# Kernel optimization log

Hardware: AMD Instinct MI355X
Metric: run time of the kernel (lower is better)

Reference implementation:

```python
import jax, jax.numpy as jnp
import numpy as np

LN_EPS = 1e-5
N, D = 512, 512


def setup_inputs() -> dict:
    key = jax.random.key(0)
    ks = jax.random.split(key, 3)
    s1 = 1.0 / np.sqrt(2 * D)  # torch Linear default-ish scale
    s2 = 1.0 / np.sqrt(D)
    return {
        "embeddings": jax.random.normal(ks[0], (N, D), jnp.float32),
        "W1": jax.random.normal(ks[1], (2 * D, D), jnp.float32) * s1,  # [in, out]
        "b1": jnp.zeros((D,), jnp.float32),
        "gamma": jnp.ones((D,), jnp.float32),
        "beta": jnp.zeros((D,), jnp.float32),
        "W2": jax.random.normal(ks[2], (D, 1), jnp.float32) * s2,
        "b2": jnp.zeros((1,), jnp.float32),
    }


def reference(embeddings, W1, b1, gamma, beta, W2, b2):
    d = embeddings.shape[-1]
    # Linear(2D -> D) on cat(e_i, e_j) decomposes into two GEMMs + broadcast add,
    # avoiding materializing the [N, N, 2D] concatenated pair tensor.
    left = embeddings @ W1[:d]              # [N, D]  (contribution of e_i)
    right = embeddings @ W1[d:] + b1        # [N, D]  (contribution of e_j + bias)
    h = left[:, None, :] + right[None, :, :]  # [N, N, D]
    # LayerNorm over last dim (eps matches torch default)
    mu = h.mean(axis=-1, keepdims=True)
    var = ((h - mu) ** 2).mean(axis=-1, keepdims=True)
    h = (h - mu) * jax.lax.rsqrt(var + LN_EPS) * gamma + beta
    # exact GELU (torch nn.GELU default)
    h = jax.nn.gelu(h, approximate=False)
    s = jax.nn.sigmoid(jnp.squeeze(h @ W2, -1) + b2[0])  # [N, N]
    # original loop only evaluates pairs i <= j and mirrors to (j, i)
    n = s.shape[0]
    upper = jnp.arange(n)[:, None] <= jnp.arange(n)[None, :]
    return jnp.where(upper, s, s.T)
```

## Files before the change

kernel.cpp:

```cpp
#include <hip/hip_runtime.h>


#define N_ 512
#define D_ 512

__global__ __launch_bounds__(256) void k_gemm(const float* __restrict__ E,
                                              const float* __restrict__ W1,
                                              const float* __restrict__ b1,
                                              float* __restrict__ W ) {
    __shared__ float e[16][516];
    const int t = threadIdx.x;
    const int cc = (blockIdx.x & 7) * 128;
    const int r0 = (blockIdx.x >> 3) * 16;
    const int half = cc >> 9;
    const int c = (cc & 511) + (t & 31) * 4;
    const int rp = (t >> 5) * 2;

    for (int x = t; x < 16 * 128; x += 256) {
        int r = x >> 7, c4 = (x & 127) << 2;
        *(float4*)&e[r][c4] = *(const float4*)&E[(r0 + r) * D_ + c4];
    }
    __syncthreads();

    const float* __restrict__ wp = W1 + (half << 18) + c;
    float4 a0 = {0.f, 0.f, 0.f, 0.f}, a1 = {0.f, 0.f, 0.f, 0.f};
#pragma unroll 4
    for (int k = 0; k < D_; k += 4) {
        float4 e0 = *(float4*)&e[rp][k];
        float4 e1 = *(float4*)&e[rp + 1][k];
        float4 wa = *(const float4*)(wp + ((k + 0) << 9));
        float4 wb = *(const float4*)(wp + ((k + 1) << 9));
        float4 wc = *(const float4*)(wp + ((k + 2) << 9));
        float4 wd = *(const float4*)(wp + ((k + 3) << 9));
        a0.x = fmaf(e0.x, wa.x, a0.x); a0.y = fmaf(e0.x, wa.y, a0.y);
        a0.z = fmaf(e0.x, wa.z, a0.z); a0.w = fmaf(e0.x, wa.w, a0.w);
        a1.x = fmaf(e1.x, wa.x, a1.x); a1.y = fmaf(e1.x, wa.y, a1.y);
        a1.z = fmaf(e1.x, wa.z, a1.z); a1.w = fmaf(e1.x, wa.w, a1.w);
        a0.x = fmaf(e0.y, wb.x, a0.x); a0.y = fmaf(e0.y, wb.y, a0.y);
        a0.z = fmaf(e0.y, wb.z, a0.z); a0.w = fmaf(e0.y, wb.w, a0.w);
        a1.x = fmaf(e1.y, wb.x, a1.x); a1.y = fmaf(e1.y, wb.y, a1.y);
        a1.z = fmaf(e1.y, wb.z, a1.z); a1.w = fmaf(e1.y, wb.w, a1.w);
        a0.x = fmaf(e0.z, wc.x, a0.x); a0.y = fmaf(e0.z, wc.y, a0.y);
        a0.z = fmaf(e0.z, wc.z, a0.z); a0.w = fmaf(e0.z, wc.w, a0.w);
        a1.x = fmaf(e1.z, wc.x, a1.x); a1.y = fmaf(e1.z, wc.y, a1.y);
        a1.z = fmaf(e1.z, wc.z, a1.z); a1.w = fmaf(e1.z, wc.w, a1.w);
        a0.x = fmaf(e0.w, wd.x, a0.x); a0.y = fmaf(e0.w, wd.y, a0.y);
        a0.z = fmaf(e0.w, wd.z, a0.z); a0.w = fmaf(e0.w, wd.w, a0.w);
        a1.x = fmaf(e1.w, wd.x, a1.x); a1.y = fmaf(e1.w, wd.y, a1.y);
        a1.z = fmaf(e1.w, wd.z, a1.z); a1.w = fmaf(e1.w, wd.w, a1.w);
    }
    if (half) {
        float4 bb = *(const float4*)(b1 + c);
        a0.x += bb.x; a0.y += bb.y; a0.z += bb.z; a0.w += bb.w;
        a1.x += bb.x; a1.y += bb.y; a1.z += bb.z; a1.w += bb.w;
    }
    *(float4*)(W + ((half << 9) + r0 + rp) * D_ + c) = a0;
    *(float4*)(W + ((half << 9) + r0 + rp + 1) * D_ + c) = a1;
}

__global__ __launch_bounds__(256) void k_center(float* __restrict__ W,
                                                float* __restrict__ var) {
    const int t = threadIdx.x;
    const int lane = t & 63;
    const int r = (blockIdx.x << 2) + (t >> 6);
    float* p = W + r * D_;
    float4 v0 = *(float4*)&p[lane << 2];
    float4 v1 = *(float4*)&p[256 + (lane << 2)];
    float s = (v0.x + v0.y) + (v0.z + v0.w) + (v1.x + v1.y) + (v1.z + v1.w);
#pragma unroll
    for (int off = 32; off > 0; off >>= 1) s += __shfl_xor(s, off, 64);
    const float mean = s * (1.f / D_);
    v0.x -= mean; v0.y -= mean; v0.z -= mean; v0.w -= mean;
    v1.x -= mean; v1.y -= mean; v1.z -= mean; v1.w -= mean;
    float ss = v0.x * v0.x + v0.y * v0.y + v0.z * v0.z + v0.w * v0.w +
               v1.x * v1.x + v1.y * v1.y + v1.z * v1.z + v1.w * v1.w;
#pragma unroll
    for (int off = 32; off > 0; off >>= 1) ss += __shfl_xor(ss, off, 64);
    *(float4*)&p[lane << 2] = v0;
    *(float4*)&p[256 + (lane << 2)] = v1;
    if (lane == 0) var[r] = ss * (1.f / D_);
}


#define GELU1(L, R, G, BE, WC, RST, ACC)                                      \
    do {                                                                      \
        float s_ = (L) + (R);                                                 \
        float x_ = fmaf(s_ * (RST), (G), (BE));                               \
        float q_ = x_ * fmaf(-0.10294340f, x_ * x_, -2.30220935f);            \
        float e_ = __builtin_amdgcn_exp2f(q_);                                \
        float ge_ = x_ * __builtin_amdgcn_rcpf(1.f + e_);                     \
        ACC = fmaf(ge_, (WC), ACC);                                           \
    } while (0)

#define GELU4(LQ, RQ, RST, ACC)                                               \
    do {                                                                      \
        GELU1(LQ.x, RQ.x, g4.x, be4.x, w4.x, RST, ACC);                       \
        GELU1(LQ.y, RQ.y, g4.y, be4.y, w4.y, RST, ACC);                       \
        GELU1(LQ.z, RQ.z, g4.z, be4.z, w4.z, RST, ACC);                       \
        GELU1(LQ.w, RQ.w, g4.w, be4.w, w4.w, RST, ACC);                       \
    } while (0)

#define DOT4(LQ, RQ, ACC)                                                     \
    ACC += LQ.x * RQ.x + LQ.y * RQ.y + LQ.z * RQ.z + LQ.w * RQ.w

#define BFLY(V)                                                               \
    do {                                                                      \
        V += __shfl_xor(V, 1, 64);                                            \
        V += __shfl_xor(V, 2, 64);                                            \
        V += __shfl_xor(V, 4, 64);                                            \
        V += __shfl_xor(V, 8, 64);                                            \
    } while (0)

__global__ __launch_bounds__(512, 4) void k_pair(const float* __restrict__ W,
                                                 const float* __restrict__ var,
                                                 const float* __restrict__ gf,
                                                 const float* __restrict__ bef,
                                                 const float* __restrict__ wf,
                                                 const float* __restrict__ b2f,
                                                 float* __restrict__ out) {
    __shared__ float ls[16][516];
    __shared__ float rs[16][516];

    const int b = blockIdx.x;
    int I = (int)((65.0f - sqrtf(4225.0f - 8.0f * (float)b)) * 0.5f);
    if (I < 0) I = 0;
    if (I > 31) I = 31;
#define S_(i) (32 * (i) - ((i) * ((i)-1)) / 2)
    while (S_(I) > b) --I;
    while (S_(I + 1) <= b) ++I;
    const int J = I + (b - S_(I));
#undef S_

    const int t = threadIdx.x;
    const int ks = t & 15;
    const int pt = t >> 4;
    const int i2 = (pt & 7) * 2, j4 = (pt >> 3) * 4;
    const int Ibase = I * 16, Jbase = N_ + J * 16;

    for (int x = t; x < 16 * 128; x += 512) {
        int r = x >> 7, c4 = (x & 127) << 2;
        *(float4*)&ls[r][c4] = *(const float4*)&W[(Ibase + r) * D_ + c4];
        *(float4*)&rs[r][c4] = *(const float4*)&W[(Jbase + r) * D_ + c4];
    }
    __syncthreads();

    float cv0 = 0.f, cv1 = 0.f, cv2 = 0.f, cv3 = 0.f;
    float cv4 = 0.f, cv5 = 0.f, cv6 = 0.f, cv7 = 0.f;
    for (int it = 0; it < 8; ++it) {
        const int kq = (it * 16 + ks) * 4;
        float4 la = *(float4*)&ls[i2][kq];
        float4 lb = *(float4*)&ls[i2 + 1][kq];
        float4 ra = *(float4*)&rs[j4][kq];
        float4 rb = *(float4*)&rs[j4 + 1][kq];
        float4 rc = *(float4*)&rs[j4 + 2][kq];
        float4 rd = *(float4*)&rs[j4 + 3][kq];
        DOT4(la, ra, cv0); DOT4(la, rb, cv1); DOT4(la, rc, cv2); DOT4(la, rd, cv3);
        DOT4(lb, ra, cv4); DOT4(lb, rb, cv5); DOT4(lb, rc, cv6); DOT4(lb, rd, cv7);
    }
    BFLY(cv0); BFLY(cv1); BFLY(cv2); BFLY(cv3);
    BFLY(cv4); BFLY(cv5); BFLY(cv6); BFLY(cv7);

    const float vl0 = var[Ibase + i2], vl1 = var[Ibase + i2 + 1];
    const float vr0 = var[Jbase + j4], vr1 = var[Jbase + j4 + 1];
    const float vr2 = var[Jbase + j4 + 2], vr3 = var[Jbase + j4 + 3];
    const float rst0 = rsqrtf(vl0 + vr0 + cv0 * (2.f / D_) + 1e-5f);
    const float rst1 = rsqrtf(vl0 + vr1 + cv1 * (2.f / D_) + 1e-5f);
    const float rst2 = rsqrtf(vl0 + vr2 + cv2 * (2.f / D_) + 1e-5f);
    const float rst3 = rsqrtf(vl0 + vr3 + cv3 * (2.f / D_) + 1e-5f);
    const float rst4 = rsqrtf(vl1 + vr0 + cv4 * (2.f / D_) + 1e-5f);
    const float rst5 = rsqrtf(vl1 + vr1 + cv5 * (2.f / D_) + 1e-5f);
    const float rst6 = rsqrtf(vl1 + vr2 + cv6 * (2.f / D_) + 1e-5f);
    const float rst7 = rsqrtf(vl1 + vr3 + cv7 * (2.f / D_) + 1e-5f);

    float ac0 = 0.f, ac1 = 0.f, ac2 = 0.f, ac3 = 0.f;
    float ac4 = 0.f, ac5 = 0.f, ac6 = 0.f, ac7 = 0.f;
    for (int it = 0; it < 8; ++it) {
        const int kq = (it * 16 + ks) * 4;
        float4 g4 = *(const float4*)&gf[kq];
        float4 be4 = *(const float4*)&bef[kq];
        float4 w4 = *(const float4*)&wf[kq];
        float4 la = *(float4*)&ls[i2][kq];
        float4 lb = *(float4*)&ls[i2 + 1][kq];
        float4 ra = *(float4*)&rs[j4][kq];
        float4 rb = *(float4*)&rs[j4 + 1][kq];
        float4 rc = *(float4*)&rs[j4 + 2][kq];
        float4 rd = *(float4*)&rs[j4 + 3][kq];
        GELU4(la, ra, rst0, ac0); GELU4(la, rb, rst1, ac1);
        GELU4(la, rc, rst2, ac2); GELU4(la, rd, rst3, ac3);
        GELU4(lb, ra, rst4, ac4); GELU4(lb, rb, rst5, ac5);
        GELU4(lb, rc, rst6, ac6); GELU4(lb, rd, rst7, ac7);
    }
    BFLY(ac0); BFLY(ac1); BFLY(ac2); BFLY(ac3);
    BFLY(ac4); BFLY(ac5); BFLY(ac6); BFLY(ac7);

    if (ks == 0) {
        const float bb = b2f[0];
        const float z0 = __builtin_amdgcn_rcpf(
            1.f + __builtin_amdgcn_exp2f(-1.44269504f * (ac0 + bb)));
        const float z1 = __builtin_amdgcn_rcpf(
            1.f + __builtin_amdgcn_exp2f(-1.44269504f * (ac1 + bb)));
        const float z2 = __builtin_amdgcn_rcpf(
            1.f + __builtin_amdgcn_exp2f(-1.44269504f * (ac2 + bb)));
        const float z3 = __builtin_amdgcn_rcpf(
            1.f + __builtin_amdgcn_exp2f(-1.44269504f * (ac3 + bb)));
        const float z4 = __builtin_amdgcn_rcpf(
            1.f + __builtin_amdgcn_exp2f(-1.44269504f * (ac4 + bb)));
        const float z5 = __builtin_amdgcn_rcpf(
            1.f + __builtin_amdgcn_exp2f(-1.44269504f * (ac5 + bb)));
        const float z6 = __builtin_amdgcn_rcpf(
            1.f + __builtin_amdgcn_exp2f(-1.44269504f * (ac6 + bb)));
        const float z7 = __builtin_amdgcn_rcpf(
            1.f + __builtin_amdgcn_exp2f(-1.44269504f * (ac7 + bb)));
        const int gi0 = Ibase + i2;
        const int gj0 = (Jbase - N_) + j4;
        if (I < J) {
            float4 o0 = {z0, z1, z2, z3};
            float4 o1 = {z4, z5, z6, z7};
            *(float4*)&out[gi0 * N_ + gj0] = o0;
            *(float4*)&out[(gi0 + 1) * N_ + gj0] = o1;
            out[gj0 * N_ + gi0] = z0;       out[gj0 * N_ + gi0 + 1] = z4;
            out[(gj0 + 1) * N_ + gi0] = z1; out[(gj0 + 1) * N_ + gi0 + 1] = z5;
            out[(gj0 + 2) * N_ + gi0] = z2; out[(gj0 + 2) * N_ + gi0 + 1] = z6;
            out[(gj0 + 3) * N_ + gi0] = z3; out[(gj0 + 3) * N_ + gi0 + 1] = z7;
        } else {
            if (gi0 <= gj0)     { out[gi0 * N_ + gj0] = z0;       out[gj0 * N_ + gi0] = z0; }
            if (gi0 <= gj0 + 1) { out[gi0 * N_ + gj0 + 1] = z1;   out[(gj0 + 1) * N_ + gi0] = z1; }
            if (gi0 <= gj0 + 2) { out[gi0 * N_ + gj0 + 2] = z2;   out[(gj0 + 2) * N_ + gi0] = z2; }
            if (gi0 <= gj0 + 3) { out[gi0 * N_ + gj0 + 3] = z3;   out[(gj0 + 3) * N_ + gi0] = z3; }
            if (gi0 + 1 <= gj0)     { out[(gi0 + 1) * N_ + gj0] = z4;     out[gj0 * N_ + gi0 + 1] = z4; }
            if (gi0 + 1 <= gj0 + 1) { out[(gi0 + 1) * N_ + gj0 + 1] = z5; out[(gj0 + 1) * N_ + gi0 + 1] = z5; }
            if (gi0 + 1 <= gj0 + 2) { out[(gi0 + 1) * N_ + gj0 + 2] = z6; out[(gj0 + 2) * N_ + gi0 + 1] = z6; }
            if (gi0 + 1 <= gj0 + 3) { out[(gi0 + 1) * N_ + gj0 + 3] = z7; out[(gj0 + 3) * N_ + gi0 + 1] = z7; }
        }
    }
}

extern "C" void kernel_launch(void* const* d_in, const int* in_sizes, int n_in,
                              void* d_out, int out_size, void* d_ws, size_t ws_size,
                              hipStream_t stream) {
    const float* E     = (const float*)d_in[0];
    const float* W1    = (const float*)d_in[1];
    const float* b1    = (const float*)d_in[2];
    const float* gamma = (const float*)d_in[3];
    const float* beta  = (const float*)d_in[4];
    const float* w2    = (const float*)d_in[5];
    const float* b2    = (const float*)d_in[6];
    float* out = (float*)d_out;

    float* F    = (float*)d_ws;
    float* lcrc = F;
    float* var  = F + 1024 * 512;

    k_gemm<<<256, 256, 0, stream>>>(E, W1, b1, lcrc);
    k_center<<<256, 256, 0, stream>>>(lcrc, var);
    k_pair<<<528, 512, 0, stream>>>(lcrc, var, gamma, beta, w2, b2, out);
}
```

Baseline: 142.6 us.

## Fuse row centering into pair kernel and widen GEMM blocks to 512 threads

Drops the separate centering kernel. The pair kernel now computes each row's mean and variance from its shared-memory tiles and folds the mean correction into the LayerNorm variance and shift terms. The GEMM now uses 512 threads per block, each computing one row instead of two, and the pair kernel's occupancy hint is lowered from 4 to 2. This saves one launch and a global read/write pass, at the cost of redundant per-block statistics, and the raw-moment variance formula is less numerically robust.

Result: slower. 148.0 us (+3.8%).

```diff
diff --git a/kernel.cpp b/kernel.cpp
--- a/kernel.cpp
+++ b/kernel.cpp
@@ -4,7 +4,7 @@
 #define N_ 512
 #define D_ 512
 
-__global__ __launch_bounds__(256) void k_gemm(const float* __restrict__ E,
+__global__ __launch_bounds__(512) void k_gemm(const float* __restrict__ E,
                                               const float* __restrict__ W1,
                                               const float* __restrict__ b1,
                                               float* __restrict__ W ) {
@@ -14,90 +14,56 @@
     const int r0 = (blockIdx.x >> 3) * 16;
     const int half = cc >> 9;
     const int c = (cc & 511) + (t & 31) * 4;
-    const int rp = (t >> 5) * 2;
-
-    for (int x = t; x < 16 * 128; x += 256) {
+    const int rp = t >> 5;
+
+    for (int x = t; x < 16 * 128; x += 512) {
         int r = x >> 7, c4 = (x & 127) << 2;
         *(float4*)&e[r][c4] = *(const float4*)&E[(r0 + r) * D_ + c4];
     }
     __syncthreads();
 
     const float* __restrict__ wp = W1 + (half << 18) + c;
-    float4 a0 = {0.f, 0.f, 0.f, 0.f}, a1 = {0.f, 0.f, 0.f, 0.f};
+    float4 a0 = {0.f, 0.f, 0.f, 0.f};
 #pragma unroll 4
     for (int k = 0; k < D_; k += 4) {
         float4 e0 = *(float4*)&e[rp][k];
-        float4 e1 = *(float4*)&e[rp + 1][k];
         float4 wa = *(const float4*)(wp + ((k + 0) << 9));
         float4 wb = *(const float4*)(wp + ((k + 1) << 9));
         float4 wc = *(const float4*)(wp + ((k + 2) << 9));
         float4 wd = *(const float4*)(wp + ((k + 3) << 9));
         a0.x = fmaf(e0.x, wa.x, a0.x); a0.y = fmaf(e0.x, wa.y, a0.y);
         a0.z = fmaf(e0.x, wa.z, a0.z); a0.w = fmaf(e0.x, wa.w, a0.w);
-        a1.x = fmaf(e1.x, wa.x, a1.x); a1.y = fmaf(e1.x, wa.y, a1.y);
-        a1.z = fmaf(e1.x, wa.z, a1.z); a1.w = fmaf(e1.x, wa.w, a1.w);
         a0.x = fmaf(e0.y, wb.x, a0.x); a0.y = fmaf(e0.y, wb.y, a0.y);
         a0.z = fmaf(e0.y, wb.z, a0.z); a0.w = fmaf(e0.y, wb.w, a0.w);
-        a1.x = fmaf(e1.y, wb.x, a1.x); a1.y = fmaf(e1.y, wb.y, a1.y);
-        a1.z = fmaf(e1.y, wb.z, a1.z); a1.w = fmaf(e1.y, wb.w, a1.w);
         a0.x = fmaf(e0.z, wc.x, a0.x); a0.y = fmaf(e0.z, wc.y, a0.y);
         a0.z = fmaf(e0.z, wc.z, a0.z); a0.w = fmaf(e0.z, wc.w, a0.w);
-        a1.x = fmaf(e1.z, wc.x, a1.x); a1.y = fmaf(e1.z, wc.y, a1.y);
-        a1.z = fmaf(e1.z, wc.z, a1.z); a1.w = fmaf(e1.z, wc.w, a1.w);
         a0.x = fmaf(e0.w, wd.x, a0.x); a0.y = fmaf(e0.w, wd.y, a0.y);
         a0.z = fmaf(e0.w, wd.z, a0.z); a0.w = fmaf(e0.w, wd.w, a0.w);
-        a1.x = fmaf(e1.w, wd.x, a1.x); a1.y = fmaf(e1.w, wd.y, a1.y);
-        a1.z = fmaf(e1.w, wd.z, a1.z); a1.w = fmaf(e1.w, wd.w, a1.w);
     }
     if (half) {
         float4 bb = *(const float4*)(b1 + c);
         a0.x += bb.x; a0.y += bb.y; a0.z += bb.z; a0.w += bb.w;
-        a1.x += bb.x; a1.y += bb.y; a1.z += bb.z; a1.w += bb.w;
     }
     *(float4*)(W + ((half << 9) + r0 + rp) * D_ + c) = a0;
-    *(float4*)(W + ((half << 9) + r0 + rp + 1) * D_ + c) = a1;
 }
 
-__global__ __launch_bounds__(256) void k_center(float* __restrict__ W,
-                                                float* __restrict__ var) {
-    const int t = threadIdx.x;
-    const int lane = t & 63;
-    const int r = (blockIdx.x << 2) + (t >> 6);
-    float* p = W + r * D_;
-    float4 v0 = *(float4*)&p[lane << 2];
-    float4 v1 = *(float4*)&p[256 + (lane << 2)];
-    float s = (v0.x + v0.y) + (v0.z + v0.w) + (v1.x + v1.y) + (v1.z + v1.w);
-#pragma unroll
-    for (int off = 32; off > 0; off >>= 1) s += __shfl_xor(s, off, 64);
-    const float mean = s * (1.f / D_);
-    v0.x -= mean; v0.y -= mean; v0.z -= mean; v0.w -= mean;
-    v1.x -= mean; v1.y -= mean; v1.z -= mean; v1.w -= mean;
-    float ss = v0.x * v0.x + v0.y * v0.y + v0.z * v0.z + v0.w * v0.w +
-               v1.x * v1.x + v1.y * v1.y + v1.z * v1.z + v1.w * v1.w;
-#pragma unroll
-    for (int off = 32; off > 0; off >>= 1) ss += __shfl_xor(ss, off, 64);
-    *(float4*)&p[lane << 2] = v0;
-    *(float4*)&p[256 + (lane << 2)] = v1;
-    if (lane == 0) var[r] = ss * (1.f / D_);
-}
-
-
-#define GELU1(L, R, G, BE, WC, RST, ACC)                                      \
+
+#define GELU1(L, R, G, BE, WC, RST, T2N, ACC)                                 \
     do {                                                                      \
         float s_ = (L) + (R);                                                 \
-        float x_ = fmaf(s_ * (RST), (G), (BE));                               \
+        float x_ = fmaf(fmaf(s_, (RST), (T2N)), (G), (BE));                   \
         float q_ = x_ * fmaf(-0.10294340f, x_ * x_, -2.30220935f);            \
         float e_ = __builtin_amdgcn_exp2f(q_);                                \
         float ge_ = x_ * __builtin_amdgcn_rcpf(1.f + e_);                     \
         ACC = fmaf(ge_, (WC), ACC);                                           \
     } while (0)
 
-#define GELU4(LQ, RQ, RST, ACC)                                               \
+#define GELU4(LQ, RQ, RST, T2N, ACC)                                          \
     do {                                                                      \
-        GELU1(LQ.x, RQ.x, g4.x, be4.x, w4.x, RST, ACC);                       \
-        GELU1(LQ.y, RQ.y, g4.y, be4.y, w4.y, RST, ACC);                       \
-        GELU1(LQ.z, RQ.z, g4.z, be4.z, w4.z, RST, ACC);                       \
-        GELU1(LQ.w, RQ.w, g4.w, be4.w, w4.w, RST, ACC);                       \
+        GELU1(LQ.x, RQ.x, g4.x, be4.x, w4.x, RST, T2N, ACC);                  \
+        GELU1(LQ.y, RQ.y, g4.y, be4.y, w4.y, RST, T2N, ACC);                  \
+        GELU1(LQ.z, RQ.z, g4.z, be4.z, w4.z, RST, T2N, ACC);                  \
+        GELU1(LQ.w, RQ.w, g4.w, be4.w, w4.w, RST, T2N, ACC);                  \
     } while (0)
 
 #define DOT4(LQ, RQ, ACC)                                                     \
@@ -111,8 +77,7 @@
         V += __shfl_xor(V, 8, 64);                                            \
     } while (0)
 
-__global__ __launch_bounds__(512, 4) void k_pair(const float* __restrict__ W,
-                                                 const float* __restrict__ var,
+__global__ __launch_bounds__(512, 2) void k_pair(const float* __restrict__ W,
                                                  const float* __restrict__ gf,
                                                  const float* __restrict__ bef,
                                                  const float* __restrict__ wf,
@@ -120,6 +85,8 @@
                                                  float* __restrict__ out) {
     __shared__ float ls[16][516];
     __shared__ float rs[16][516];
+    __shared__ float smean[32];
+    __shared__ float svar[32];
 
     const int b = blockIdx.x;
     int I = (int)((65.0f - sqrtf(4225.0f - 8.0f * (float)b)) * 0.5f);
@@ -141,6 +108,31 @@
         int r = x >> 7, c4 = (x & 127) << 2;
         *(float4*)&ls[r][c4] = *(const float4*)&W[(Ibase + r) * D_ + c4];
         *(float4*)&rs[r][c4] = *(const float4*)&W[(Jbase + r) * D_ + c4];
+    }
+    __syncthreads();
+
+    {
+        const int lane = t & 63, w = t >> 6;
+#pragma unroll
+        for (int rr = 0; rr < 4; ++rr) {
+            const int row = w * 4 + rr;
+            const float* p = (row < 16) ? &ls[row][0] : &rs[row - 16][0];
+            float4 a = *(const float4*)&p[lane << 2];
+            float4 c = *(const float4*)&p[256 + (lane << 2)];
+            float sm = (a.x + a.y) + (a.z + a.w) + (c.x + c.y) + (c.z + c.w);
+            float sq = a.x * a.x + a.y * a.y + a.z * a.z + a.w * a.w +
+                       c.x * c.x + c.y * c.y + c.z * c.z + c.w * c.w;
+#pragma unroll
+            for (int off = 32; off > 0; off >>= 1) {
+                sm += __shfl_xor(sm, off, 64);
+                sq += __shfl_xor(sq, off, 64);
+            }
+            if (lane == 0) {
+                float mu = sm * (1.f / D_);
+                smean[row] = mu;
+                svar[row] = fmaf(-mu, mu, sq * (1.f / D_));
+            }
+        }
     }
     __syncthreads();
 
@@ -160,17 +152,28 @@
     BFLY(cv0); BFLY(cv1); BFLY(cv2); BFLY(cv3);
     BFLY(cv4); BFLY(cv5); BFLY(cv6); BFLY(cv7);
 
-    const float vl0 = var[Ibase + i2], vl1 = var[Ibase + i2 + 1];
-    const float vr0 = var[Jbase + j4], vr1 = var[Jbase + j4 + 1];
-    const float vr2 = var[Jbase + j4 + 2], vr3 = var[Jbase + j4 + 3];
-    const float rst0 = rsqrtf(vl0 + vr0 + cv0 * (2.f / D_) + 1e-5f);
-    const float rst1 = rsqrtf(vl0 + vr1 + cv1 * (2.f / D_) + 1e-5f);
-    const float rst2 = rsqrtf(vl0 + vr2 + cv2 * (2.f / D_) + 1e-5f);
-    const float rst3 = rsqrtf(vl0 + vr3 + cv3 * (2.f / D_) + 1e-5f);
-    const float rst4 = rsqrtf(vl1 + vr0 + cv4 * (2.f / D_) + 1e-5f);
-    const float rst5 = rsqrtf(vl1 + vr1 + cv5 * (2.f / D_) + 1e-5f);
-    const float rst6 = rsqrtf(vl1 + vr2 + cv6 * (2.f / D_) + 1e-5f);
-    const float rst7 = rsqrtf(vl1 + vr3 + cv7 * (2.f / D_) + 1e-5f);
+    const float ml0 = smean[i2], ml1 = smean[i2 + 1];
+    const float vl0 = svar[i2], vl1 = svar[i2 + 1];
+    const float mr0 = smean[16 + j4],     mr1 = smean[16 + j4 + 1];
+    const float mr2 = smean[16 + j4 + 2], mr3 = smean[16 + j4 + 3];
+    const float vr0 = svar[16 + j4],     vr1 = svar[16 + j4 + 1];
+    const float vr2 = svar[16 + j4 + 2], vr3 = svar[16 + j4 + 3];
+    const float rst0 = rsqrtf(vl0 + vr0 + cv0 * (2.f / D_) - 2.f * ml0 * mr0 + 1e-5f);
+    const float rst1 = rsqrtf(vl0 + vr1 + cv1 * (2.f / D_) - 2.f * ml0 * mr1 + 1e-5f);
+    const float rst2 = rsqrtf(vl0 + vr2 + cv2 * (2.f / D_) - 2.f * ml0 * mr2 + 1e-5f);
+    const float rst3 = rsqrtf(vl0 + vr3 + cv3 * (2.f / D_) - 2.f * ml0 * mr3 + 1e-5f);
+    const float rst4 = rsqrtf(vl1 + vr0 + cv4 * (2.f / D_) - 2.f * ml1 * mr0 + 1e-5f);
+    const float rst5 = rsqrtf(vl1 + vr1 + cv5 * (2.f / D_) - 2.f * ml1 * mr1 + 1e-5f);
+    const float rst6 = rsqrtf(vl1 + vr2 + cv6 * (2.f / D_) - 2.f * ml1 * mr2 + 1e-5f);
+    const float rst7 = rsqrtf(vl1 + vr3 + cv7 * (2.f / D_) - 2.f * ml1 * mr3 + 1e-5f);
+    const float t2n0 = -(ml0 + mr0) * rst0;
+    const float t2n1 = -(ml0 + mr1) * rst1;
+    const float t2n2 = -(ml0 + mr2) * rst2;
+    const float t2n3 = -(ml0 + mr3) * rst3;
+    const float t2n4 = -(ml1 + mr0) * rst4;
+    const float t2n5 = -(ml1 + mr1) * rst5;
+    const float t2n6 = -(ml1 + mr2) * rst6;
+    const float t2n7 = -(ml1 + mr3) * rst7;
 
     float ac0 = 0.f, ac1 = 0.f, ac2 = 0.f, ac3 = 0.f;
     float ac4 = 0.f, ac5 = 0.f, ac6 = 0.f, ac7 = 0.f;
@@ -185,10 +188,10 @@
         float4 rb = *(float4*)&rs[j4 + 1][kq];
         float4 rc = *(float4*)&rs[j4 + 2][kq];
         float4 rd = *(float4*)&rs[j4 + 3][kq];
-        GELU4(la, ra, rst0, ac0); GELU4(la, rb, rst1, ac1);
-        GELU4(la, rc, rst2, ac2); GELU4(la, rd, rst3, ac3);
-        GELU4(lb, ra, rst4, ac4); GELU4(lb, rb, rst5, ac5);
-        GELU4(lb, rc, rst6, ac6); GELU4(lb, rd, rst7, ac7);
+        GELU4(la, ra, rst0, t2n0, ac0); GELU4(la, rb, rst1, t2n1, ac1);
+        GELU4(la, rc, rst2, t2n2, ac2); GELU4(la, rd, rst3, t2n3, ac3);
+        GELU4(lb, ra, rst4, t2n4, ac4); GELU4(lb, rb, rst5, t2n5, ac5);
+        GELU4(lb, rc, rst6, t2n6, ac6); GELU4(lb, rd, rst7, t2n7, ac7);
     }
     BFLY(ac0); BFLY(ac1); BFLY(ac2); BFLY(ac3);
     BFLY(ac4); BFLY(ac5); BFLY(ac6); BFLY(ac7);
@@ -247,11 +250,8 @@
     const float* b2    = (const float*)d_in[6];
     float* out = (float*)d_out;
 
-    float* F    = (float*)d_ws;
-    float* lcrc = F;
-    float* var  = F + 1024 * 512;
-
-    k_gemm<<<256, 256, 0, stream>>>(E, W1, b1, lcrc);
-    k_center<<<256, 256, 0, stream>>>(lcrc, var);
-    k_pair<<<528, 512, 0, stream>>>(lcrc, var, gamma, beta, w2, b2, out);
+    float* lcrc = (float*)d_ws;
+
+    k_gemm<<<256, 512, 0, stream>>>(E, W1, b1, lcrc);
+    k_pair<<<528, 512, 0, stream>>>(lcrc, gamma, beta, w2, b2, out);
 }
```
